# Optimization experiments

Hardware: AMD Instinct MI355X
Metric: run time of the kernel (lower is better)

Reference implementation:

```python
import jax, jax.numpy as jnp
import numpy as np

B, T, TOKEN_DIM, TPR_DIM = 16, 256, 256, 10
INNER = TOKEN_DIM // 4  # 64
TH = 32                 # tpr_mlp hidden dim
EPS = 1e-5              # BatchNorm eps


def _bn(x, g, b, m, v):
    # BatchNorm1d in eval mode: normalize with running stats
    return (x - m) * jax.lax.rsqrt(v + EPS) * g + b


def setup_inputs() -> dict:
    key = jax.random.key(0)
    ks = iter(jax.random.split(key, 32))
    def n(shape, s=0.02):
        return jax.random.normal(next(ks), shape, dtype=jnp.float32) * s
    def bn_params(c):
        g = 1.0 + 0.1 * jax.random.normal(next(ks), (c,), dtype=jnp.float32)
        b = 0.1 * jax.random.normal(next(ks), (c,), dtype=jnp.float32)
        m = 0.1 * jax.random.normal(next(ks), (c,), dtype=jnp.float32)
        v = jax.random.uniform(next(ks), (c,), dtype=jnp.float32, minval=0.5, maxval=1.5)
        return g, b, m, v
    inp = {}
    inp['x'] = jax.random.normal(next(ks), (B, T, TOKEN_DIM), dtype=jnp.float32)
    inp['r'] = jax.random.normal(next(ks), (B, T, T, TPR_DIM), dtype=jnp.float32)
    # fc1: Linear(token,token) + BN(token)
    inp['W1'] = n((TOKEN_DIM, TOKEN_DIM)); inp['b1'] = n((TOKEN_DIM,))
    inp['bn1_g'], inp['bn1_b'], inp['bn1_m'], inp['bn1_v'] = bn_params(TOKEN_DIM)
    # VectorAttention
    inp['Wqkv'] = n((TOKEN_DIM, 3 * INNER))
    inp['Wt1'] = n((TPR_DIM, TH)); inp['bt1'] = n((TH,))
    inp['bnt_g'], inp['bnt_b'], inp['bnt_m'], inp['bnt_v'] = bn_params(TH)
    inp['Wt2'] = n((TH, INNER)); inp['bt2'] = n((INNER,))
    inp['Wa1'] = n((INNER, INNER)); inp['ba1'] = n((INNER,))
    inp['Wa2'] = n((INNER, INNER)); inp['ba2'] = n((INNER,))
    # fc2: Linear(inner, token) + BN(token)
    inp['W2'] = n((INNER, TOKEN_DIM)); inp['b2'] = n((TOKEN_DIM,))
    inp['bn2_g'], inp['bn2_b'], inp['bn2_m'], inp['bn2_v'] = bn_params(TOKEN_DIM)
    return inp


def reference(x, r, W1, b1, bn1_g, bn1_b, bn1_m, bn1_v, Wqkv,
              Wt1, bt1, bnt_g, bnt_b, bnt_m, bnt_v, Wt2, bt2,
              Wa1, ba1, Wa2, ba2, W2, b2, bn2_g, bn2_b, bn2_m, bn2_v):
    # fc1 + BN, residual skip (pre-relu)
    y = _bn(x @ W1 + b1, bn1_g, bn1_b, bn1_m, bn1_v)  # [B,T,C]
    skip = y
    y = jax.nn.relu(y)
    # VectorAttention
    qkv = y @ Wqkv                                     # [B,T,3*inner]
    q, k, v = jnp.split(qkv, 3, axis=-1)               # each [B,T,inner]
    qk_rel = q[:, :, None, :] - k[:, None, :, :]       # [B,T,T,inner]
    rel_emb = jax.nn.relu(_bn(r @ Wt1 + bt1, bnt_g, bnt_b, bnt_m, bnt_v)) @ Wt2 + bt2  # [B,T,T,inner]
    vv = v[:, None, :, :] + rel_emb                    # [B,T,T,inner]
    h = jax.nn.relu((qk_rel + rel_emb) @ Wa1 + ba1)
    sim = h @ Wa2 + ba2                                # [B,T,T,inner]
    attn = jax.nn.softmax(sim, axis=-2)                # softmax over j (neighbor) axis
    agg = jnp.sum(attn * vv, axis=2)                   # [B,T,inner]
    # fc2 + BN + residual + relu
    out = jax.nn.relu(_bn(agg @ W2 + b2, bn2_g, bn2_b, bn2_m, bn2_v) + skip)
    return out  # [B,T,token_dim]
```

## Files before the change

kernel.cpp:

```cpp
#include <hip/hip_runtime.h>
#include <hip/hip_bf16.h>
#include <math.h>

#define BB 16
#define TT 256
#define CC 256
#define INNER 64
#define TPR 10
#define THD 32
#define EPSV 1e-5f

typedef __attribute__((ext_vector_type(8))) short short8;
typedef __attribute__((ext_vector_type(4))) float f32x4;
typedef __attribute__((ext_vector_type(4))) unsigned int u32x4;

__device__ __forceinline__ short f2bf(float f) {
    unsigned u = __float_as_uint(f);
    u += 0x7fffu + ((u >> 16) & 1);
    return (short)(u >> 16);
}
__device__ __forceinline__ unsigned cvtpk(float a, float b) {
    __hip_bfloat162 h = __float22bfloat162_rn(float2{a, b});
    return *(unsigned*)&h;
}
__device__ __forceinline__ float bf_lo(unsigned u) { return __uint_as_float(u << 16); }
__device__ __forceinline__ float bf_hi(unsigned u) { return __uint_as_float(u & 0xffff0000u); }

#define IMG_WT1  0
#define IMG_WT2  2048
#define IMG_WA1  6144
#define IMG_WA2  14336
#define IMG_C1   22528
#define IMG_SZ   22656

__device__ __forceinline__ int sww(int pb, int key) {
    return ((pb & ~15) ^ key) | (pb & 15);
}

__global__ __launch_bounds__(256) void prep_kernel(
    const float* __restrict__ Wt1, const float* __restrict__ bt1,
    const float* __restrict__ gt, const float* __restrict__ bbt,
    const float* __restrict__ mt, const float* __restrict__ vt,
    const float* __restrict__ Wt2, const float* __restrict__ Wa1,
    const float* __restrict__ Wa2, char* __restrict__ img)
{
    const int blk = blockIdx.x, t = threadIdx.x;
    if (blk == 0) {
        for (int e = t; e < 32 * 32; e += 256) {
            int m = e >> 5, k = e & 31;
            float scv = gt[m] * rsqrtf(vt[m] + EPSV);
            float v = (k < TPR) ? Wt1[k * 32 + m] * scv : 0.f;
            *(short*)(img + IMG_WT1 + m * 64 + k * 2) = f2bf(v);
        }
        if (t < 32) {
            float scv = gt[t] * rsqrtf(vt[t] + EPSV);
            ((float*)(img + IMG_C1))[t] = (bt1[t] - mt[t]) * scv + bbt[t];
        }
    } else if (blk == 1) {
        for (int e = t; e < 32 * 64; e += 256) {
            int h = e >> 6, c = e & 63;
            int off = IMG_WT2 + (c >> 1) * 128 + sww((c & 1) * 64 + h * 2, ((c >> 1) & 7) << 4);
            *(short*)(img + off) = f2bf(Wt2[e]);
        }
    } else {
        const float* W = (blk == 2) ? Wa1 : Wa2;
        int base = (blk == 2) ? IMG_WA1 : IMG_WA2;
        for (int e = t; e < 64 * 64; e += 256) {
            int k = e >> 6, c = e & 63;
            int off = base + c * 128 + sww(k * 2, (c & 7) << 4);
            *(short*)(img + off) = f2bf(W[e]);
        }
    }
}

__global__ __launch_bounds__(256) void fc1_qkv_kernel(
    const float* __restrict__ x, const float* __restrict__ W1, const float* __restrict__ b1,
    const float* __restrict__ g1, const float* __restrict__ bb1,
    const float* __restrict__ m1, const float* __restrict__ v1,
    const float* __restrict__ Wqkv,
    float* __restrict__ skip, float* __restrict__ qkv)
{
    const int ROWS = 8;
    __shared__ float xr[ROWS][CC];
    __shared__ float yr[ROWS][CC];
    const int n0 = blockIdx.x * ROWS;
    const int t = threadIdx.x;

#pragma unroll
    for (int rr = 0; rr < ROWS; ++rr)
        xr[rr][t] = x[(size_t)(n0 + rr) * CC + t];
    __syncthreads();

    float acc[ROWS];
#pragma unroll
    for (int rr = 0; rr < ROWS; ++rr) acc[rr] = 0.f;
    for (int k = 0; k < CC; ++k) {
        float wv = W1[(size_t)k * CC + t];
#pragma unroll
        for (int rr = 0; rr < ROWS; ++rr) acc[rr] = fmaf(xr[rr][k], wv, acc[rr]);
    }
    const float s1 = g1[t] * rsqrtf(v1[t] + EPSV);
    const float base = b1[t] - m1[t];
    const float bet = bb1[t];
#pragma unroll
    for (int rr = 0; rr < ROWS; ++rr) {
        float y = (acc[rr] + base) * s1 + bet;
        skip[(size_t)(n0 + rr) * CC + t] = y;
        yr[rr][t] = fmaxf(y, 0.f);
    }
    __syncthreads();

    if (t < 192) {
        float a2[ROWS];
#pragma unroll
        for (int rr = 0; rr < ROWS; ++rr) a2[rr] = 0.f;
        for (int k = 0; k < CC; ++k) {
            float wv = Wqkv[(size_t)k * 192 + t];
#pragma unroll
            for (int rr = 0; rr < ROWS; ++rr) a2[rr] = fmaf(yr[rr][k], wv, a2[rr]);
        }
#pragma unroll
        for (int rr = 0; rr < ROWS; ++rr)
            qkv[(size_t)(n0 + rr) * 192 + t] = a2[rr];
    }
}

#define O_R    0
#define O_TH   20480
#define O_WT1  53248
#define O_WT2  55296
#define O_WA1  59392
#define O_WA2  67584
#define O_RED  75776
#define LDSZ   79872

__device__ __forceinline__ int swb(int row, int cb, int sh, int mask) {
    return (row << sh) + (((cb & ~15) ^ ((row & mask) << 4)) | (cb & 15));
}
__device__ __forceinline__ short8 ldfrag(const char* lds, int base, int row, int cb16, int sh, int mask) {
    return *(const short8*)(lds + base + (row << sh) + (cb16 ^ ((row & mask) << 4)));
}

__global__ __launch_bounds__(512, 2) void attn_mfma_kernel(
    const float* __restrict__ r, const float* __restrict__ qkv,
    const float* __restrict__ bt2, const float* __restrict__ ba1,
    const char* __restrict__ img, float* __restrict__ agg)
{
    __shared__ __align__(16) char lds[LDSZ];
    const int n = blockIdx.x, b = n >> 8;
    const int tid = threadIdx.x;
    const int wv = tid >> 6, lane = tid & 63;
    const int lid = lane & 15, q4 = lane >> 4;
    const int kb = q4 * 16;
    const int jt0 = wv * 2;

    const float* kvb = qkv + (size_t)b * (TT * 192);
    const f32x4 z4 = {0.f, 0.f, 0.f, 0.f};

#pragma unroll
    for (int ci = 0; ci < 3; ++ci) {
        int c = wv + ci * 8;
        if (c < 22) {
            int ldsoff;
            if (c < 2)       ldsoff = O_WT1 + c * 1024;
            else if (c < 6)  ldsoff = O_WT2 + (c - 2) * 1024;
            else if (c < 14) ldsoff = O_WA1 + (c - 6) * 1024;
            else             ldsoff = O_WA2 + (c - 14) * 1024;
            __builtin_amdgcn_global_load_lds(
                (const __attribute__((address_space(1))) unsigned*)(const unsigned*)(img + c * 1024 + lane * 16),
                (__attribute__((address_space(3))) unsigned*)(unsigned*)(lds + ldsoff + lane * 16),
                16, 0, 0);
        }
    }

    f32x4 qv4[4], k4[4][2];
#pragma unroll
    for (int tm = 0; tm < 4; ++tm) {
        int ch0 = tm * 16 + q4 * 4;
        qv4[tm] = *(const f32x4*)(qkv + (size_t)n * 192 + ch0);
#pragma unroll
        for (int tn = 0; tn < 2; ++tn) {
            int j = (jt0 + tn) * 16 + lid;
            k4[tm][tn] = *(const f32x4*)(kvb + (size_t)j * 192 + 64 + ch0);
        }
    }

    {
        const float* rrow = r + (size_t)n * (TT * TPR);
        int j = tid >> 1, hf = tid & 1;
        const float* rp = rrow + j * TPR + hf * 5;
        float v0 = rp[0], v1 = rp[1], v2 = rp[2], v3 = rp[3], v4 = rp[4];
        float o0 = __shfl_xor(v0, 1);
        float o1 = __shfl_xor(v1, 1);
        float o2 = __shfl_xor(v2, 1);
        char* rb = lds + O_R + j * 80;
        u32x4 z = {0u, 0u, 0u, 0u};
        if (hf == 0) {
            u32x4 c;
            c[0] = cvtpk(v0, v1); c[1] = cvtpk(v2, v3);
            c[2] = cvtpk(v4, o0); c[3] = cvtpk(o1, o2);
            *(u32x4*)(rb) = c;
            *(u32x4*)(rb + 32) = z;
        } else {
            u32x4 c;
            c[0] = cvtpk(v3, v4); c[1] = 0u; c[2] = 0u; c[3] = 0u;
            *(u32x4*)(rb + 16) = c;
            *(u32x4*)(rb + 48) = z;
        }
    }
    __syncthreads();

    const float* c1g = (const float*)(img + IMG_C1);

    {
        short8 a10 = *(const short8*)(lds + O_WT1 + lid * 64 + kb);
        short8 a11 = *(const short8*)(lds + O_WT1 + (16 + lid) * 64 + kb);
        f32x4 c1v0 = *(const f32x4*)(c1g + q4 * 4);
        f32x4 c1v1 = *(const f32x4*)(c1g + 16 + q4 * 4);
        f32x4 acc1[2][2];
#pragma unroll
        for (int tn = 0; tn < 2; ++tn) {
            int j = (jt0 + tn) * 16 + lid;
            short8 bf = *(const short8*)(lds + O_R + j * 80 + kb);
            acc1[0][tn] = __builtin_amdgcn_mfma_f32_16x16x32_bf16(a10, bf, c1v0, 0, 0, 0);
            acc1[1][tn] = __builtin_amdgcn_mfma_f32_16x16x32_bf16(a11, bf, c1v1, 0, 0, 0);
        }
#pragma unroll
        for (int tm = 0; tm < 2; ++tm)
#pragma unroll
            for (int tn = 0; tn < 2; ++tn) {
                int j = (jt0 + tn) * 16 + lid;
                uint2 w;
                w.x = cvtpk(fmaxf(acc1[tm][tn][0], 0.f), fmaxf(acc1[tm][tn][1], 0.f));
                w.y = cvtpk(fmaxf(acc1[tm][tn][2], 0.f), fmaxf(acc1[tm][tn][3], 0.f));
                *(uint2*)(lds + O_TH + swb(j, tm * 32 + q4 * 8, 7, 7)) = w;
            }
    }

    uint2 pk[4][2];
#pragma unroll
    for (int tm = 0; tm < 4; ++tm)
#pragma unroll
        for (int tn = 0; tn < 2; ++tn) {
            pk[tm][tn].x = cvtpk(qv4[tm][0] - k4[tm][tn][0], qv4[tm][1] - k4[tm][tn][1]);
            pk[tm][tn].y = cvtpk(qv4[tm][2] - k4[tm][tn][2], qv4[tm][3] - k4[tm][tn][3]);
        }

    f32x4 v4h[4][2], bt2v[4];
#pragma unroll
    for (int tm = 0; tm < 4; ++tm) {
        int ch0 = tm * 16 + q4 * 4;
        bt2v[tm] = *(const f32x4*)(bt2 + ch0);
#pragma unroll
        for (int tn = 0; tn < 2; ++tn) {
            int j = (jt0 + tn) * 16 + lid;
            v4h[tm][tn] = *(const f32x4*)(kvb + (size_t)j * 192 + 128 + ch0);
        }
    }

    f32x4 rel[4][2];
    {
        short8 aw[4];
#pragma unroll
        for (int tm = 0; tm < 4; ++tm) {
            int c = tm * 16 + lid;
            aw[tm] = ldfrag(lds, O_WT2, c >> 1, (c & 1) * 64 + kb, 7, 7);
        }
#pragma unroll
        for (int tn = 0; tn < 2; ++tn) {
            int j = (jt0 + tn) * 16 + lid;
            short8 bf = ldfrag(lds, O_TH, j, kb, 7, 7);
#pragma unroll
            for (int tm = 0; tm < 4; ++tm)
                rel[tm][tn] = __builtin_amdgcn_mfma_f32_16x16x32_bf16(aw[tm], bf, bt2v[tm], 0, 0, 0);
        }
    }

    uint2 vvp[4][2];
#pragma unroll
    for (int tm = 0; tm < 4; ++tm)
#pragma unroll
        for (int tn = 0; tn < 2; ++tn) {
            int j = (jt0 + tn) * 16 + lid;
            float r0 = rel[tm][tn][0], r1 = rel[tm][tn][1];
            float r2 = rel[tm][tn][2], r3 = rel[tm][tn][3];
            float t0 = bf_lo(pk[tm][tn].x) + r0;
            float t1 = bf_hi(pk[tm][tn].x) + r1;
            float t2 = bf_lo(pk[tm][tn].y) + r2;
            float t3 = bf_hi(pk[tm][tn].y) + r3;
            uint2 w; w.x = cvtpk(t0, t1); w.y = cvtpk(t2, t3);
            *(uint2*)(lds + O_TH + swb(j, tm * 32 + q4 * 8, 7, 7)) = w;
            vvp[tm][tn].x = cvtpk(v4h[tm][tn][0] + r0, v4h[tm][tn][1] + r1);
            vvp[tm][tn].y = cvtpk(v4h[tm][tn][2] + r2, v4h[tm][tn][3] + r3);
        }

    f32x4 ba1v[4];
#pragma unroll
    for (int tm = 0; tm < 4; ++tm)
        ba1v[tm] = *(const f32x4*)(ba1 + tm * 16 + q4 * 4);
    f32x4 acc[4][2];
#pragma unroll
    for (int tm = 0; tm < 4; ++tm)
#pragma unroll
        for (int tn = 0; tn < 2; ++tn) acc[tm][tn] = ba1v[tm];
#pragma unroll
    for (int ks = 0; ks < 2; ++ks) {
        short8 aw[4];
#pragma unroll
        for (int tm = 0; tm < 4; ++tm)
            aw[tm] = ldfrag(lds, O_WA1, tm * 16 + lid, ks * 64 + kb, 7, 7);
#pragma unroll
        for (int tn = 0; tn < 2; ++tn) {
            int j = (jt0 + tn) * 16 + lid;
            short8 bf = ldfrag(lds, O_TH, j, ks * 64 + kb, 7, 7);
#pragma unroll
            for (int tm = 0; tm < 4; ++tm)
                acc[tm][tn] = __builtin_amdgcn_mfma_f32_16x16x32_bf16(aw[tm], bf, acc[tm][tn], 0, 0, 0);
        }
    }
#pragma unroll
    for (int tm = 0; tm < 4; ++tm)
#pragma unroll
        for (int tn = 0; tn < 2; ++tn) {
            int j = (jt0 + tn) * 16 + lid;
            uint2 w;
            w.x = cvtpk(fmaxf(acc[tm][tn][0], 0.f), fmaxf(acc[tm][tn][1], 0.f));
            w.y = cvtpk(fmaxf(acc[tm][tn][2], 0.f), fmaxf(acc[tm][tn][3], 0.f));
            *(uint2*)(lds + O_TH + swb(j, tm * 32 + q4 * 8, 7, 7)) = w;
        }

#pragma unroll
    for (int tm = 0; tm < 4; ++tm)
#pragma unroll
        for (int tn = 0; tn < 2; ++tn) acc[tm][tn] = z4;
#pragma unroll
    for (int ks = 0; ks < 2; ++ks) {
        short8 aw[4];
#pragma unroll
        for (int tm = 0; tm < 4; ++tm)
            aw[tm] = ldfrag(lds, O_WA2, tm * 16 + lid, ks * 64 + kb, 7, 7);
#pragma unroll
        for (int tn = 0; tn < 2; ++tn) {
            int j = (jt0 + tn) * 16 + lid;
            short8 bf = ldfrag(lds, O_TH, j, ks * 64 + kb, 7, 7);
#pragma unroll
            for (int tm = 0; tm < 4; ++tm)
                acc[tm][tn] = __builtin_amdgcn_mfma_f32_16x16x32_bf16(aw[tm], bf, acc[tm][tn], 0, 0, 0);
        }
    }

#pragma unroll
    for (int tm = 0; tm < 4; ++tm) {
        f32x4 num = z4, den = z4;
#pragma unroll
        for (int tn = 0; tn < 2; ++tn) {
            float vf0 = bf_lo(vvp[tm][tn].x), vf1 = bf_hi(vvp[tm][tn].x);
            float vf2 = bf_lo(vvp[tm][tn].y), vf3 = bf_hi(vvp[tm][tn].y);
            float e0 = __expf(acc[tm][tn][0]);
            float e1 = __expf(acc[tm][tn][1]);
            float e2 = __expf(acc[tm][tn][2]);
            float e3 = __expf(acc[tm][tn][3]);
            den[0] += e0; num[0] = fmaf(e0, vf0, num[0]);
            den[1] += e1; num[1] = fmaf(e1, vf1, num[1]);
            den[2] += e2; num[2] = fmaf(e2, vf2, num[2]);
            den[3] += e3; num[3] = fmaf(e3, vf3, num[3]);
        }
#pragma unroll
        for (int ofs = 1; ofs < 16; ofs <<= 1) {
#pragma unroll
            for (int g = 0; g < 4; ++g) {
                num[g] += __shfl_xor(num[g], ofs);
                den[g] += __shfl_xor(den[g], ofs);
            }
        }
        if (lid == 0) {
            int base = O_RED + ((wv * 4 + tm) * 4 + q4) * 32;
            *(f32x4*)(lds + base) = num;
            *(f32x4*)(lds + base + 16) = den;
        }
    }
    __syncthreads();

    if (tid < 64) {
        int tm = tid >> 4, qq = (tid >> 2) & 3, g = tid & 3;
        float nn = 0.f, dd = 0.f;
#pragma unroll
        for (int w = 0; w < 8; ++w) {
            int base = O_RED + ((w * 4 + tm) * 4 + qq) * 32 + g * 4;
            nn += *(const float*)(lds + base);
            dd += *(const float*)(lds + base + 16);
        }
        agg[(size_t)n * 64 + tid] = nn / dd;
    }
}

__global__ __launch_bounds__(256) void fc2_kernel(
    const float* __restrict__ agg, const float* __restrict__ W2, const float* __restrict__ b2,
    const float* __restrict__ g2, const float* __restrict__ bb2,
    const float* __restrict__ m2, const float* __restrict__ v2,
    const float* __restrict__ skip, float* __restrict__ out)
{
    const int ROWS = 8;
    __shared__ float ar[ROWS][INNER];
    const int n0 = blockIdx.x * ROWS;
    const int t = threadIdx.x;

    for (int idx = t; idx < ROWS * INNER; idx += 256)
        ((float*)ar)[idx] = agg[(size_t)n0 * INNER + idx];
    __syncthreads();

    const float s2 = g2[t] * rsqrtf(v2[t] + EPSV);
    const float base = b2[t] - m2[t];
    const float bet = bb2[t];

    float accv[ROWS];
#pragma unroll
    for (int rr = 0; rr < ROWS; ++rr) accv[rr] = 0.f;
    for (int k = 0; k < INNER; ++k) {
        float wv = W2[(size_t)k * CC + t];
#pragma unroll
        for (int rr = 0; rr < ROWS; ++rr) accv[rr] = fmaf(ar[rr][k], wv, accv[rr]);
    }
#pragma unroll
    for (int rr = 0; rr < ROWS; ++rr) {
        float y = (accv[rr] + base) * s2 + bet;
        out[(size_t)(n0 + rr) * CC + t] =
            fmaxf(y + skip[(size_t)(n0 + rr) * CC + t], 0.f);
    }
}

extern "C" void kernel_launch(void* const* d_in, const int* in_sizes, int n_in,
                              void* d_out, int out_size, void* d_ws, size_t ws_size,
                              hipStream_t stream)
{
    const float* x   = (const float*)d_in[0];
    const float* r   = (const float*)d_in[1];
    const float* W1  = (const float*)d_in[2];
    const float* b1  = (const float*)d_in[3];
    const float* g1  = (const float*)d_in[4];
    const float* bb1 = (const float*)d_in[5];
    const float* m1  = (const float*)d_in[6];
    const float* v1  = (const float*)d_in[7];
    const float* Wqkv= (const float*)d_in[8];
    const float* Wt1 = (const float*)d_in[9];
    const float* bt1 = (const float*)d_in[10];
    const float* gt  = (const float*)d_in[11];
    const float* bbt = (const float*)d_in[12];
    const float* mt  = (const float*)d_in[13];
    const float* vt  = (const float*)d_in[14];
    const float* Wt2 = (const float*)d_in[15];
    const float* bt2 = (const float*)d_in[16];
    const float* Wa1 = (const float*)d_in[17];
    const float* ba1 = (const float*)d_in[18];
    const float* Wa2 = (const float*)d_in[19];
    const float* W2  = (const float*)d_in[21];
    const float* b2  = (const float*)d_in[22];
    const float* g2  = (const float*)d_in[23];
    const float* bb2 = (const float*)d_in[24];
    const float* m2  = (const float*)d_in[25];
    const float* v2  = (const float*)d_in[26];
    float* out = (float*)d_out;

    const int N = BB * TT;
    float* skip = (float*)d_ws;
    float* qkv  = skip + (size_t)N * CC;
    float* agg  = qkv  + (size_t)N * 192;
    char*  img  = (char*)(agg + (size_t)N * 64);

    prep_kernel<<<dim3(4), dim3(256), 0, stream>>>(
        Wt1, bt1, gt, bbt, mt, vt, Wt2, Wa1, Wa2, img);
    fc1_qkv_kernel<<<dim3(N / 8), dim3(256), 0, stream>>>(
        x, W1, b1, g1, bb1, m1, v1, Wqkv, skip, qkv);
    attn_mfma_kernel<<<dim3(N), dim3(512), 0, stream>>>(
        r, qkv, bt2, ba1, img, agg);
    fc2_kernel<<<dim3(N / 8), dim3(256), 0, stream>>>(
        agg, W2, b2, g2, bb2, m2, v2, skip, out);
}
```

Before: 181.0 us.

## Read weights and r from global, shrink LDS, raise occupancy to four blocks

Weight fragments (Wt2, Wa1, Wa2, Wt1) are now read straight from the global prep image in unswizzled layouts instead of being staged into LDS. The r tile is loaded directly into MFMA B-operand registers instead of passing through LDS, which removes a barrier. LDS use drops to the hidden-activation tile plus the reduction area, and launch bounds ask for four blocks per CU instead of two. q and bt2 are folded into the MFMA accumulator init, and v-q-bt2 is precomputed so that vv and qk+rel come from one MFMA result. The cost is repeated global/L2 fragment loads per wave and a tighter register budget.

After: 234.1 us. 1.29x slower.

```diff
diff --git a/kernel.cpp b/kernel.cpp
--- a/kernel.cpp
+++ b/kernel.cpp
@@ -32,10 +32,6 @@
 #define IMG_WA2  14336
 #define IMG_C1   22528
 #define IMG_SZ   22656
-
-__device__ __forceinline__ int sww(int pb, int key) {
-    return ((pb & ~15) ^ key) | (pb & 15);
-}
 
 __global__ __launch_bounds__(256) void prep_kernel(
     const float* __restrict__ Wt1, const float* __restrict__ bt1,
@@ -59,16 +55,14 @@
     } else if (blk == 1) {
         for (int e = t; e < 32 * 64; e += 256) {
             int h = e >> 6, c = e & 63;
-            int off = IMG_WT2 + (c >> 1) * 128 + sww((c & 1) * 64 + h * 2, ((c >> 1) & 7) << 4);
-            *(short*)(img + off) = f2bf(Wt2[e]);
+            *(short*)(img + IMG_WT2 + c * 64 + h * 2) = f2bf(Wt2[e]);
         }
     } else {
         const float* W = (blk == 2) ? Wa1 : Wa2;
         int base = (blk == 2) ? IMG_WA1 : IMG_WA2;
         for (int e = t; e < 64 * 64; e += 256) {
             int k = e >> 6, c = e & 63;
-            int off = base + c * 128 + sww(k * 2, (c & 7) << 4);
-            *(short*)(img + off) = f2bf(W[e]);
+            *(short*)(img + base + c * 128 + k * 2) = f2bf(W[e]);
         }
     }
 }
@@ -125,23 +119,18 @@
     }
 }
 
-#define O_R    0
-#define O_TH   20480
-#define O_WT1  53248
-#define O_WT2  55296
-#define O_WA1  59392
-#define O_WA2  67584
-#define O_RED  75776
-#define LDSZ   79872
-
-__device__ __forceinline__ int swb(int row, int cb, int sh, int mask) {
-    return (row << sh) + (((cb & ~15) ^ ((row & mask) << 4)) | (cb & 15));
-}
-__device__ __forceinline__ short8 ldfrag(const char* lds, int base, int row, int cb16, int sh, int mask) {
-    return *(const short8*)(lds + base + (row << sh) + (cb16 ^ ((row & mask) << 4)));
-}
-
-__global__ __launch_bounds__(512, 2) void attn_mfma_kernel(
+#define O_TH   0
+#define O_RED  32768
+#define LDSZ   36864
+
+__device__ __forceinline__ int swb(int row, int cb) {
+    return (row << 7) + (((cb & ~15) ^ ((row & 7) << 4)) | (cb & 15));
+}
+__device__ __forceinline__ short8 ldTH(const char* lds, int row, int cb16) {
+    return *(const short8*)(lds + O_TH + (row << 7) + (cb16 ^ ((row & 7) << 4)));
+}
+
+__global__ __launch_bounds__(512, 4) void attn_mfma_kernel(
     const float* __restrict__ r, const float* __restrict__ qkv,
     const float* __restrict__ bt2, const float* __restrict__ ba1,
     const char* __restrict__ img, float* __restrict__ agg)
@@ -157,73 +146,54 @@
     const float* kvb = qkv + (size_t)b * (TT * 192);
     const f32x4 z4 = {0.f, 0.f, 0.f, 0.f};
 
-#pragma unroll
-    for (int ci = 0; ci < 3; ++ci) {
-        int c = wv + ci * 8;
-        if (c < 22) {
-            int ldsoff;
-            if (c < 2)       ldsoff = O_WT1 + c * 1024;
-            else if (c < 6)  ldsoff = O_WT2 + (c - 2) * 1024;
-            else if (c < 14) ldsoff = O_WA1 + (c - 6) * 1024;
-            else             ldsoff = O_WA2 + (c - 14) * 1024;
-            __builtin_amdgcn_global_load_lds(
-                (const __attribute__((address_space(1))) unsigned*)(const unsigned*)(img + c * 1024 + lane * 16),
-                (__attribute__((address_space(3))) unsigned*)(unsigned*)(lds + ldsoff + lane * 16),
-                16, 0, 0);
-        }
-    }
-
-    f32x4 qv4[4], k4[4][2];
+    f32x4 cbv[4];
 #pragma unroll
     for (int tm = 0; tm < 4; ++tm) {
         int ch0 = tm * 16 + q4 * 4;
-        qv4[tm] = *(const f32x4*)(qkv + (size_t)n * 192 + ch0);
+        f32x4 qv = *(const f32x4*)(qkv + (size_t)n * 192 + ch0);
+        f32x4 bv = *(const f32x4*)(bt2 + ch0);
+#pragma unroll
+        for (int g = 0; g < 4; ++g) cbv[tm][g] = qv[g] + bv[g];
+    }
+    uint2 wp[4][2];
+#pragma unroll
+    for (int tm = 0; tm < 4; ++tm) {
+        int ch0 = tm * 16 + q4 * 4;
 #pragma unroll
         for (int tn = 0; tn < 2; ++tn) {
             int j = (jt0 + tn) * 16 + lid;
-            k4[tm][tn] = *(const f32x4*)(kvb + (size_t)j * 192 + 64 + ch0);
+            f32x4 v4 = *(const f32x4*)(kvb + (size_t)j * 192 + 128 + ch0);
+            wp[tm][tn].x = cvtpk(v4[0] - cbv[tm][0], v4[1] - cbv[tm][1]);
+            wp[tm][tn].y = cvtpk(v4[2] - cbv[tm][2], v4[3] - cbv[tm][3]);
         }
     }
 
     {
-        const float* rrow = r + (size_t)n * (TT * TPR);
-        int j = tid >> 1, hf = tid & 1;
-        const float* rp = rrow + j * TPR + hf * 5;
-        float v0 = rp[0], v1 = rp[1], v2 = rp[2], v3 = rp[3], v4 = rp[4];
-        float o0 = __shfl_xor(v0, 1);
-        float o1 = __shfl_xor(v1, 1);
-        float o2 = __shfl_xor(v2, 1);
-        char* rb = lds + O_R + j * 80;
-        u32x4 z = {0u, 0u, 0u, 0u};
-        if (hf == 0) {
-            u32x4 c;
-            c[0] = cvtpk(v0, v1); c[1] = cvtpk(v2, v3);
-            c[2] = cvtpk(v4, o0); c[3] = cvtpk(o1, o2);
-            *(u32x4*)(rb) = c;
-            *(u32x4*)(rb + 32) = z;
-        } else {
-            u32x4 c;
-            c[0] = cvtpk(v3, v4); c[1] = 0u; c[2] = 0u; c[3] = 0u;
-            *(u32x4*)(rb + 16) = c;
-            *(u32x4*)(rb + 48) = z;
-        }
-    }
-    __syncthreads();
-
-    const float* c1g = (const float*)(img + IMG_C1);
-
-    {
-        short8 a10 = *(const short8*)(lds + O_WT1 + lid * 64 + kb);
-        short8 a11 = *(const short8*)(lds + O_WT1 + (16 + lid) * 64 + kb);
+        short8 a10 = *(const short8*)(img + IMG_WT1 + lid * 64 + kb);
+        short8 a11 = *(const short8*)(img + IMG_WT1 + (16 + lid) * 64 + kb);
+        const float* c1g = (const float*)(img + IMG_C1);
         f32x4 c1v0 = *(const f32x4*)(c1g + q4 * 4);
         f32x4 c1v1 = *(const f32x4*)(c1g + 16 + q4 * 4);
         f32x4 acc1[2][2];
 #pragma unroll
         for (int tn = 0; tn < 2; ++tn) {
             int j = (jt0 + tn) * 16 + lid;
-            short8 bf = *(const short8*)(lds + O_R + j * 80 + kb);
-            acc1[0][tn] = __builtin_amdgcn_mfma_f32_16x16x32_bf16(a10, bf, c1v0, 0, 0, 0);
-            acc1[1][tn] = __builtin_amdgcn_mfma_f32_16x16x32_bf16(a11, bf, c1v1, 0, 0, 0);
+            const float* rj = r + (size_t)n * (TT * TPR) + j * TPR;
+            union { short8 s; u32x4 u; } bb;
+            bb.u[0] = 0u; bb.u[1] = 0u; bb.u[2] = 0u; bb.u[3] = 0u;
+            if (q4 == 0) {
+                float2 a0 = *(const float2*)(rj);
+                float2 a1 = *(const float2*)(rj + 2);
+                float2 a2 = *(const float2*)(rj + 4);
+                float2 a3 = *(const float2*)(rj + 6);
+                bb.u[0] = cvtpk(a0.x, a0.y); bb.u[1] = cvtpk(a1.x, a1.y);
+                bb.u[2] = cvtpk(a2.x, a2.y); bb.u[3] = cvtpk(a3.x, a3.y);
+            } else if (q4 == 1) {
+                float2 a0 = *(const float2*)(rj + 8);
+                bb.u[0] = cvtpk(a0.x, a0.y);
+            }
+            acc1[0][tn] = __builtin_amdgcn_mfma_f32_16x16x32_bf16(a10, bb.s, c1v0, 0, 0, 0);
+            acc1[1][tn] = __builtin_amdgcn_mfma_f32_16x16x32_bf16(a11, bb.s, c1v1, 0, 0, 0);
         }
 #pragma unroll
         for (int tm = 0; tm < 2; ++tm)
@@ -233,89 +203,71 @@
                 uint2 w;
                 w.x = cvtpk(fmaxf(acc1[tm][tn][0], 0.f), fmaxf(acc1[tm][tn][1], 0.f));
                 w.y = cvtpk(fmaxf(acc1[tm][tn][2], 0.f), fmaxf(acc1[tm][tn][3], 0.f));
-                *(uint2*)(lds + O_TH + swb(j, tm * 32 + q4 * 8, 7, 7)) = w;
-            }
-    }
-
-    uint2 pk[4][2];
-#pragma unroll
-    for (int tm = 0; tm < 4; ++tm)
-#pragma unroll
-        for (int tn = 0; tn < 2; ++tn) {
-            pk[tm][tn].x = cvtpk(qv4[tm][0] - k4[tm][tn][0], qv4[tm][1] - k4[tm][tn][1]);
-            pk[tm][tn].y = cvtpk(qv4[tm][2] - k4[tm][tn][2], qv4[tm][3] - k4[tm][tn][3]);
-        }
-
-    f32x4 v4h[4][2], bt2v[4];
+                *(uint2*)(lds + swb(j, tm * 32 + q4 * 8)) = w;
+            }
+    }
+
+    uint2 vvp[4][2];
+    {
+        short8 bfh[2];
+#pragma unroll
+        for (int tn = 0; tn < 2; ++tn)
+            bfh[tn] = ldTH(lds, (jt0 + tn) * 16 + lid, kb);
+#pragma unroll
+        for (int hf = 0; hf < 2; ++hf) {
+            const int tA = hf * 2, tB = hf * 2 + 1;
+            short8 awA = *(const short8*)(img + IMG_WT2 + (tA * 16 + lid) * 64 + kb);
+            short8 awB = *(const short8*)(img + IMG_WT2 + (tB * 16 + lid) * 64 + kb);
+            f32x4 kA[2], kB[2];
+#pragma unroll
+            for (int tn = 0; tn < 2; ++tn) {
+                int j = (jt0 + tn) * 16 + lid;
+                kA[tn] = *(const f32x4*)(kvb + (size_t)j * 192 + 64 + tA * 16 + q4 * 4);
+                kB[tn] = *(const f32x4*)(kvb + (size_t)j * 192 + 64 + tB * 16 + q4 * 4);
+            }
+            f32x4 rA[2], rB[2];
+#pragma unroll
+            for (int tn = 0; tn < 2; ++tn) {
+                rA[tn] = __builtin_amdgcn_mfma_f32_16x16x32_bf16(awA, bfh[tn], cbv[tA], 0, 0, 0);
+                rB[tn] = __builtin_amdgcn_mfma_f32_16x16x32_bf16(awB, bfh[tn], cbv[tB], 0, 0, 0);
+            }
+#pragma unroll
+            for (int tn = 0; tn < 2; ++tn) {
+                int j = (jt0 + tn) * 16 + lid;
+                uint2 w;
+                w.x = cvtpk(rA[tn][0] - kA[tn][0], rA[tn][1] - kA[tn][1]);
+                w.y = cvtpk(rA[tn][2] - kA[tn][2], rA[tn][3] - kA[tn][3]);
+                *(uint2*)(lds + swb(j, tA * 32 + q4 * 8)) = w;
+                w.x = cvtpk(rB[tn][0] - kB[tn][0], rB[tn][1] - kB[tn][1]);
+                w.y = cvtpk(rB[tn][2] - kB[tn][2], rB[tn][3] - kB[tn][3]);
+                *(uint2*)(lds + swb(j, tB * 32 + q4 * 8)) = w;
+                vvp[tA][tn].x = cvtpk(bf_lo(wp[tA][tn].x) + rA[tn][0], bf_hi(wp[tA][tn].x) + rA[tn][1]);
+                vvp[tA][tn].y = cvtpk(bf_lo(wp[tA][tn].y) + rA[tn][2], bf_hi(wp[tA][tn].y) + rA[tn][3]);
+                vvp[tB][tn].x = cvtpk(bf_lo(wp[tB][tn].x) + rB[tn][0], bf_hi(wp[tB][tn].x) + rB[tn][1]);
+                vvp[tB][tn].y = cvtpk(bf_lo(wp[tB][tn].y) + rB[tn][2], bf_hi(wp[tB][tn].y) + rB[tn][3]);
+            }
+        }
+    }
+
+    f32x4 acc[4][2];
 #pragma unroll
     for (int tm = 0; tm < 4; ++tm) {
-        int ch0 = tm * 16 + q4 * 4;
-        bt2v[tm] = *(const f32x4*)(bt2 + ch0);
-#pragma unroll
-        for (int tn = 0; tn < 2; ++tn) {
-            int j = (jt0 + tn) * 16 + lid;
-            v4h[tm][tn] = *(const f32x4*)(kvb + (size_t)j * 192 + 128 + ch0);
-        }
-    }
-
-    f32x4 rel[4][2];
-    {
-        short8 aw[4];
-#pragma unroll
-        for (int tm = 0; tm < 4; ++tm) {
-            int c = tm * 16 + lid;
-            aw[tm] = ldfrag(lds, O_WT2, c >> 1, (c & 1) * 64 + kb, 7, 7);
-        }
-#pragma unroll
-        for (int tn = 0; tn < 2; ++tn) {
-            int j = (jt0 + tn) * 16 + lid;
-            short8 bf = ldfrag(lds, O_TH, j, kb, 7, 7);
-#pragma unroll
-            for (int tm = 0; tm < 4; ++tm)
-                rel[tm][tn] = __builtin_amdgcn_mfma_f32_16x16x32_bf16(aw[tm], bf, bt2v[tm], 0, 0, 0);
-        }
-    }
-
-    uint2 vvp[4][2];
-#pragma unroll
-    for (int tm = 0; tm < 4; ++tm)
-#pragma unroll
-        for (int tn = 0; tn < 2; ++tn) {
-            int j = (jt0 + tn) * 16 + lid;
-            float r0 = rel[tm][tn][0], r1 = rel[tm][tn][1];
-            float r2 = rel[tm][tn][2], r3 = rel[tm][tn][3];
-            float t0 = bf_lo(pk[tm][tn].x) + r0;
-            float t1 = bf_hi(pk[tm][tn].x) + r1;
-            float t2 = bf_lo(pk[tm][tn].y) + r2;
-            float t3 = bf_hi(pk[tm][tn].y) + r3;
-            uint2 w; w.x = cvtpk(t0, t1); w.y = cvtpk(t2, t3);
-            *(uint2*)(lds + O_TH + swb(j, tm * 32 + q4 * 8, 7, 7)) = w;
-            vvp[tm][tn].x = cvtpk(v4h[tm][tn][0] + r0, v4h[tm][tn][1] + r1);
-            vvp[tm][tn].y = cvtpk(v4h[tm][tn][2] + r2, v4h[tm][tn][3] + r3);
-        }
-
-    f32x4 ba1v[4];
-#pragma unroll
-    for (int tm = 0; tm < 4; ++tm)
-        ba1v[tm] = *(const f32x4*)(ba1 + tm * 16 + q4 * 4);
-    f32x4 acc[4][2];
-#pragma unroll
-    for (int tm = 0; tm < 4; ++tm)
-#pragma unroll
-        for (int tn = 0; tn < 2; ++tn) acc[tm][tn] = ba1v[tm];
+        f32x4 bv = *(const f32x4*)(ba1 + tm * 16 + q4 * 4);
+#pragma unroll
+        for (int tn = 0; tn < 2; ++tn) acc[tm][tn] = bv;
+    }
 #pragma unroll
     for (int ks = 0; ks < 2; ++ks) {
         short8 aw[4];
 #pragma unroll
         for (int tm = 0; tm < 4; ++tm)
-            aw[tm] = ldfrag(lds, O_WA1, tm * 16 + lid, ks * 64 + kb, 7, 7);
-#pragma unroll
-        for (int tn = 0; tn < 2; ++tn) {
-            int j = (jt0 + tn) * 16 + lid;
-            short8 bf = ldfrag(lds, O_TH, j, ks * 64 + kb, 7, 7);
+            aw[tm] = *(const short8*)(img + IMG_WA1 + (tm * 16 + lid) * 128 + ks * 64 + kb);
+#pragma unroll
+        for (int tn = 0; tn < 2; ++tn) {
+            short8 bt = ldTH(lds, (jt0 + tn) * 16 + lid, ks * 64 + kb);
 #pragma unroll
             for (int tm = 0; tm < 4; ++tm)
-                acc[tm][tn] = __builtin_amdgcn_mfma_f32_16x16x32_bf16(aw[tm], bf, acc[tm][tn], 0, 0, 0);
+                acc[tm][tn] = __builtin_amdgcn_mfma_f32_16x16x32_bf16(aw[tm], bt, acc[tm][tn], 0, 0, 0);
         }
     }
 #pragma unroll
@@ -326,7 +278,7 @@
             uint2 w;
             w.x = cvtpk(fmaxf(acc[tm][tn][0], 0.f), fmaxf(acc[tm][tn][1], 0.f));
             w.y = cvtpk(fmaxf(acc[tm][tn][2], 0.f), fmaxf(acc[tm][tn][3], 0.f));
-            *(uint2*)(lds + O_TH + swb(j, tm * 32 + q4 * 8, 7, 7)) = w;
+            *(uint2*)(lds + swb(j, tm * 32 + q4 * 8)) = w;
         }
 
 #pragma unroll
@@ -338,14 +290,13 @@
         short8 aw[4];
 #pragma unroll
         for (int tm = 0; tm < 4; ++tm)
-            aw[tm] = ldfrag(lds, O_WA2, tm * 16 + lid, ks * 64 + kb, 7, 7);
-#pragma unroll
-        for (int tn = 0; tn < 2; ++tn) {
-            int j = (jt0 + tn) * 16 + lid;
-            short8 bf = ldfrag(lds, O_TH, j, ks * 64 + kb, 7, 7);
+            aw[tm] = *(const short8*)(img + IMG_WA2 + (tm * 16 + lid) * 128 + ks * 64 + kb);
+#pragma unroll
+        for (int tn = 0; tn < 2; ++tn) {
+            short8 bt = ldTH(lds, (jt0 + tn) * 16 + lid, ks * 64 + kb);
 #pragma unroll
             for (int tm = 0; tm < 4; ++tm)
-                acc[tm][tn] = __builtin_amdgcn_mfma_f32_16x16x32_bf16(aw[tm], bf, acc[tm][tn], 0, 0, 0);
+                acc[tm][tn] = __builtin_amdgcn_mfma_f32_16x16x32_bf16(aw[tm], bt, acc[tm][tn], 0, 0, 0);
         }
     }
 
```
